# Optimization experiments

Hardware: AMD Instinct MI355X
Metric: run time of the kernel (lower is better)

Reference implementation:

```python
import jax, jax.numpy as jnp
import numpy as np

N_NODES = 100000
N_EDGES = 1250000
D_IN = 64
D_OUT = 64


def setup_inputs() -> dict:
    key = jax.random.key(0)
    k1, k2, k3, k4, k5, k6 = jax.random.split(key, 6)
    x = jax.random.normal(k1, (N_NODES, D_IN), dtype=jnp.float32)
    W_self = jax.random.normal(k2, (D_IN, D_OUT), dtype=jnp.float32) / np.sqrt(D_IN)
    W_neigh = jax.random.normal(k3, (D_IN, D_OUT), dtype=jnp.float32) / np.sqrt(D_IN)
    b = jax.random.normal(k4, (D_OUT,), dtype=jnp.float32) * 0.01
    src = jax.random.randint(k5, (N_EDGES,), 0, N_NODES, dtype=jnp.int32)
    dst = jnp.sort(jax.random.randint(k6, (N_EDGES,), 0, N_NODES, dtype=jnp.int32))
    return {"x": x, "W_self": W_self, "W_neigh": W_neigh, "b": b, "src": src, "dst": dst}


def reference(x, W_self, W_neigh, b, src, dst):
    # DGL SAGEConv (aggregator_type='mean'):
    #   h_neigh[v] = mean_{u in N(v)} x[u]   (0 if in-degree 0)
    #   out = x @ W_self + h_neigh @ W_neigh + b
    n_nodes = x.shape[0]
    msgs = x[src]  # [E, D_IN] gather of source features
    agg = jax.ops.segment_sum(msgs, dst, num_segments=n_nodes)  # [N, D_IN]
    deg = jax.ops.segment_sum(jnp.ones_like(dst, dtype=x.dtype), dst, num_segments=n_nodes)
    h_neigh = agg / jnp.maximum(deg, 1.0)[:, None]
    return x @ W_self + h_neigh @ W_neigh + b
```

## Files before the change

### kernel.cpp

```cpp
#include <hip/hip_runtime.h>
#include <hip/hip_fp16.h>

#define NN 100000
#define NE 1250000
#define D 64
#define NTILE 1563
#define NWID (NTILE * 4)

__device__ inline float2 cvt2(unsigned u) {
    __half2 h = __builtin_bit_cast(__half2, u);
    return __half22float2(h);
}
__device__ inline unsigned pack2(float a, float b) {
    __half2 h = __floats2half2_rn(a, b);
    return __builtin_bit_cast(unsigned, h);
}

__global__ __launch_bounds__(256) void k_rowptr(const int* __restrict__ dst,
                                                int* __restrict__ row_ptr) {
    const int i = blockIdx.x * 256 + threadIdx.x;
    if (i >= NE) return;
    const int d = dst[i];
    const int prev = (i == 0) ? -1 : dst[i - 1];
    for (int v = prev + 1; v <= d; ++v) row_ptr[v] = i;
    if (i == NE - 1) {
        for (int v = d + 1; v <= NN; ++v) row_ptr[v] = NE;
    }
}

__global__ __launch_bounds__(256) void k_gemm(const float* __restrict__ x,
                                              const float* __restrict__ Wself,
                                              const float* __restrict__ Wneigh,
                                              const float* __restrict__ b,
                                              float* __restrict__ z,
                                              __half* __restrict__ y) {
    const int lane = threadIdx.x & 63;
    const int wid = __builtin_amdgcn_readfirstlane(blockIdx.x * 4 + (threadIdx.x >> 6));
    if (wid >= NWID) return;
    const int tile = wid >> 2;
    const int sel = wid & 3;
    const int jh = (sel & 1) * 32;
    const float* __restrict__ W = (sel & 2) ? Wneigh : Wself;

    const int n = tile * 64 + lane;
    const int nc = (n < NN) ? n : (NN - 1);
    const float* __restrict__ xr = x + (size_t)nc * D;

    float acc[32];
    #pragma unroll
    for (int j = 0; j < 32; ++j) acc[j] = 0.0f;

    #pragma unroll 2
    for (int k4 = 0; k4 < D / 4; ++k4) {
        const float4 xv = *(const float4*)(xr + k4 * 4);
        const float xk[4] = {xv.x, xv.y, xv.z, xv.w};
        #pragma unroll
        for (int i = 0; i < 4; ++i) {
            const float* __restrict__ wr = W + (k4 * 4 + i) * D + jh;
            #pragma unroll
            for (int j = 0; j < 32; ++j) {
                acc[j] = fmaf(xk[i], wr[j], acc[j]);
            }
        }
    }

    if (n < NN) {
        if (sel & 2) {
            unsigned p[16];
            #pragma unroll
            for (int g = 0; g < 16; ++g) p[g] = pack2(acc[2 * g], acc[2 * g + 1]);
            uint4* __restrict__ yo = (uint4*)(y + (size_t)n * D + jh);
            #pragma unroll
            for (int g = 0; g < 4; ++g) {
                uint4 v;
                v.x = p[4 * g + 0]; v.y = p[4 * g + 1];
                v.z = p[4 * g + 2]; v.w = p[4 * g + 3];
                yo[g] = v;
            }
        } else {
            float* __restrict__ zo = z + (size_t)n * D + jh;
            const float* __restrict__ br = b + jh;
            #pragma unroll
            for (int g = 0; g < 8; ++g) {
                float4 v;
                v.x = acc[g * 4 + 0] + br[g * 4 + 0];
                v.y = acc[g * 4 + 1] + br[g * 4 + 1];
                v.z = acc[g * 4 + 2] + br[g * 4 + 2];
                v.w = acc[g * 4 + 3] + br[g * 4 + 3];
                *(float4*)(zo + g * 4) = v;
            }
        }
    }
}

__global__ __launch_bounds__(256) void k_aggr(const __half* __restrict__ y,
                                              const int* __restrict__ src,
                                              const int* __restrict__ row_ptr,
                                              float* __restrict__ out) {
    const int lane = threadIdx.x & 63;
    const int half = lane >> 5;
    const int w    = lane & 31;
    const int wid  = blockIdx.x * 4 + (threadIdx.x >> 6);
    const int v    = wid * 2 + half;
    if (v >= NN) return;

    const int lo = row_ptr[v];
    const int hi = row_ptr[v + 1];
    const int deg = hi - lo;

    float a0 = 0.0f, a1 = 0.0f;
    if (deg > 0) {
        const int last = hi - 1;
        int sv[4];
        #pragma unroll
        for (int u = 0; u < 4; ++u) sv[u] = src[min(lo + u, last)];
        for (int e = lo; e < hi; e += 4) {
            unsigned r[4];
            #pragma unroll
            for (int u = 0; u < 4; ++u)
                r[u] = *(const unsigned*)(y + (size_t)sv[u] * D + w * 2);
            const int en = e + 4;
            #pragma unroll
            for (int u = 0; u < 4; ++u) sv[u] = src[min(en + u, last)];
            #pragma unroll
            for (int u = 0; u < 4; ++u) {
                if (e + u < hi) {
                    const float2 f = cvt2(r[u]);
                    a0 += f.x; a1 += f.y;
                }
            }
        }
    }
    const float inv = (deg > 0) ? 1.0f / (float)deg : 0.0f;
    float2* op = (float2*)(out + (size_t)v * D + w * 2);
    float2 o = *op;
    o.x += a0 * inv;
    o.y += a1 * inv;
    *op = o;
}

extern "C" void kernel_launch(void* const* d_in, const int* in_sizes, int n_in,
                              void* d_out, int out_size, void* d_ws, size_t ws_size,
                              hipStream_t stream) {
    const float* x      = (const float*)d_in[0];
    const float* Wself  = (const float*)d_in[1];
    const float* Wneigh = (const float*)d_in[2];
    const float* b      = (const float*)d_in[3];
    const int*   src    = (const int*)d_in[4];
    const int*   dst    = (const int*)d_in[5];
    float* out = (float*)d_out;

    __half* y      = (__half*)d_ws;
    int*   row_ptr = (int*)((char*)d_ws + (size_t)NN * D * 2);

    k_rowptr<<<(NE + 255) / 256, 256, 0, stream>>>(dst, row_ptr);
    k_gemm<<<(NWID + 3) / 4, 256, 0, stream>>>(x, Wself, Wneigh, b, out, y);
    k_aggr<<<(NN + 7) / 8, 256, 0, stream>>>(y, src, row_ptr, out);
}
```

Measured before the change: 154.8 us.

## Use split-fp16 MFMA for dense projection with pre-packed weights

```diff
diff --git a/kernel.cpp b/kernel.cpp
--- a/kernel.cpp
+++ b/kernel.cpp
@@ -4,91 +4,104 @@
 #define NN 100000
 #define NE 1250000
 #define D 64
-#define NTILE 1563
-#define NWID (NTILE * 4)
+#define MT 6250
+#define RP_BLOCKS 4883
+
+typedef _Float16 h8 __attribute__((ext_vector_type(8)));
+typedef float f4 __attribute__((ext_vector_type(4)));
 
 __device__ inline float2 cvt2(unsigned u) {
     __half2 h = __builtin_bit_cast(__half2, u);
     return __half22float2(h);
 }
-__device__ inline unsigned pack2(float a, float b) {
-    __half2 h = __floats2half2_rn(a, b);
-    return __builtin_bit_cast(unsigned, h);
-}
 
-__global__ __launch_bounds__(256) void k_rowptr(const int* __restrict__ dst,
-                                                int* __restrict__ row_ptr) {
-    const int i = blockIdx.x * 256 + threadIdx.x;
-    if (i >= NE) return;
-    const int d = dst[i];
-    const int prev = (i == 0) ? -1 : dst[i - 1];
-    for (int v = prev + 1; v <= d; ++v) row_ptr[v] = i;
-    if (i == NE - 1) {
-        for (int v = d + 1; v <= NN; ++v) row_ptr[v] = NE;
+__global__ __launch_bounds__(256) void k_prep(const int* __restrict__ dst,
+                                              int* __restrict__ row_ptr,
+                                              const float* __restrict__ Ws,
+                                              const float* __restrict__ Wn,
+                                              __half* __restrict__ Wp) {
+    if (blockIdx.x < RP_BLOCKS) {
+        const int i = blockIdx.x * 256 + threadIdx.x;
+        if (i >= NE) return;
+        const int d = dst[i];
+        const int prev = (i == 0) ? -1 : dst[i - 1];
+        for (int v = prev + 1; v <= d; ++v) row_ptr[v] = i;
+        if (i == NE - 1) {
+            for (int v = d + 1; v <= NN; ++v) row_ptr[v] = NE;
+        }
+    } else {
+        const int id = (blockIdx.x - RP_BLOCKS) * 256 + threadIdx.x;
+        const int p = id >> 13;
+        const int r = id & 8191;
+        const int i = r & 7;
+        const int l = (r >> 3) & 63;
+        const int f = (r >> 9) & 1;
+        const int t = r >> 10;
+        const int k = f * 32 + ((l >> 4) * 8) + i;
+        const int c = (t & 3) * 16 + (l & 15);
+        const float v = ((t < 4) ? Ws : Wn)[k * D + c];
+        const _Float16 hi = (_Float16)v;
+        const _Float16 out = p ? (_Float16)(v - (float)hi) : hi;
+        Wp[p * 8192 + r] = __builtin_bit_cast(__half, out);
     }
 }
 
-__global__ __launch_bounds__(256) void k_gemm(const float* __restrict__ x,
-                                              const float* __restrict__ Wself,
-                                              const float* __restrict__ Wneigh,
-                                              const float* __restrict__ b,
-                                              float* __restrict__ z,
-                                              __half* __restrict__ y) {
+__global__ __launch_bounds__(256) void k_mm(const float* __restrict__ x,
+                                            const __half* __restrict__ Wp,
+                                            const float* __restrict__ b,
+                                            float* __restrict__ z,
+                                            __half* __restrict__ y) {
     const int lane = threadIdx.x & 63;
-    const int wid = __builtin_amdgcn_readfirstlane(blockIdx.x * 4 + (threadIdx.x >> 6));
-    if (wid >= NWID) return;
-    const int tile = wid >> 2;
-    const int sel = wid & 3;
-    const int jh = (sel & 1) * 32;
-    const float* __restrict__ W = (sel & 2) ? Wneigh : Wself;
+    const int mt = blockIdx.x * 4 + (threadIdx.x >> 6);
+    if (mt >= MT) return;
+    const int row = lane & 15;
+    const int kg = lane >> 4;
+    const float* __restrict__ xr = x + (size_t)(mt * 16 + row) * D + kg * 8;
 
-    const int n = tile * 64 + lane;
-    const int nc = (n < NN) ? n : (NN - 1);
-    const float* __restrict__ xr = x + (size_t)nc * D;
+    const float4 v0 = *(const float4*)(xr);
+    const float4 v1 = *(const float4*)(xr + 4);
+    const float4 v2 = *(const float4*)(xr + 32);
+    const float4 v3 = *(const float4*)(xr + 36);
 
-    float acc[32];
+    const float xf0[8] = {v0.x, v0.y, v0.z, v0.w, v1.x, v1.y, v1.z, v1.w};
+    const float xf1[8] = {v2.x, v2.y, v2.z, v2.w, v3.x, v3.y, v3.z, v3.w};
+    h8 ah0, al0, ah1, al1;
     #pragma unroll
-    for (int j = 0; j < 32; ++j) acc[j] = 0.0f;
-
-    #pragma unroll 2
-    for (int k4 = 0; k4 < D / 4; ++k4) {
-        const float4 xv = *(const float4*)(xr + k4 * 4);
-        const float xk[4] = {xv.x, xv.y, xv.z, xv.w};
-        #pragma unroll
-        for (int i = 0; i < 4; ++i) {
-            const float* __restrict__ wr = W + (k4 * 4 + i) * D + jh;
-            #pragma unroll
-            for (int j = 0; j < 32; ++j) {
-                acc[j] = fmaf(xk[i], wr[j], acc[j]);
-            }
-        }
+    for (int i = 0; i < 8; ++i) {
+        const _Float16 h0 = (_Float16)xf0[i];
+        ah0[i] = h0;
+        al0[i] = (_Float16)(xf0[i] - (float)h0);
+        const _Float16 h1 = (_Float16)xf1[i];
+        ah1[i] = h1;
+        al1[i] = (_Float16)(xf1[i] - (float)h1);
     }
 
-    if (n < NN) {
-        if (sel & 2) {
-            unsigned p[16];
+    const _Float16* __restrict__ wp = (const _Float16*)Wp;
+    #pragma unroll
+    for (int t = 0; t < 8; ++t) {
+        const h8 bh0 = *(const h8*)(wp + ((t * 2 + 0) * 64 + lane) * 8);
+        const h8 bh1 = *(const h8*)(wp + ((t * 2 + 1) * 64 + lane) * 8);
+        const h8 bl0 = *(const h8*)(wp + 8192 + ((t * 2 + 0) * 64 + lane) * 8);
+        const h8 bl1 = *(const h8*)(wp + 8192 + ((t * 2 + 1) * 64 + lane) * 8);
+        f4 acc = {0.f, 0.f, 0.f, 0.f};
+        acc = __builtin_amdgcn_mfma_f32_16x16x32_f16(al0, bh0, acc, 0, 0, 0);
+        acc = __builtin_amdgcn_mfma_f32_16x16x32_f16(al1, bh1, acc, 0, 0, 0);
+        acc = __builtin_amdgcn_mfma_f32_16x16x32_f16(ah0, bl0, acc, 0, 0, 0);
+        acc = __builtin_amdgcn_mfma_f32_16x16x32_f16(ah1, bl1, acc, 0, 0, 0);
+        acc = __builtin_amdgcn_mfma_f32_16x16x32_f16(ah0, bh0, acc, 0, 0, 0);
+        acc = __builtin_amdgcn_mfma_f32_16x16x32_f16(ah1, bh1, acc, 0, 0, 0);
+
+        const int col = (t & 3) * 16 + (lane & 15);
+        const int r0 = mt * 16 + kg * 4;
+        if (t < 4) {
+            const float bb = b[col];
             #pragma unroll
-            for (int g = 0; g < 16; ++g) p[g] = pack2(acc[2 * g], acc[2 * g + 1]);
-            uint4* __restrict__ yo = (uint4*)(y + (size_t)n * D + jh);
+            for (int reg = 0; reg < 4; ++reg)
+                z[(size_t)(r0 + reg) * D + col] = acc[reg] + bb;
+        } else {
             #pragma unroll
-            for (int g = 0; g < 4; ++g) {
-                uint4 v;
-                v.x = p[4 * g + 0]; v.y = p[4 * g + 1];
-                v.z = p[4 * g + 2]; v.w = p[4 * g + 3];
-                yo[g] = v;
-            }
-        } else {
-            float* __restrict__ zo = z + (size_t)n * D + jh;
-            const float* __restrict__ br = b + jh;
-            #pragma unroll
-            for (int g = 0; g < 8; ++g) {
-                float4 v;
-                v.x = acc[g * 4 + 0] + br[g * 4 + 0];
-                v.y = acc[g * 4 + 1] + br[g * 4 + 1];
-                v.z = acc[g * 4 + 2] + br[g * 4 + 2];
-                v.w = acc[g * 4 + 3] + br[g * 4 + 3];
-                *(float4*)(zo + g * 4) = v;
-            }
+            for (int reg = 0; reg < 4; ++reg)
+                y[(size_t)(r0 + reg) * D + col] = __float2half(acc[reg]);
         }
     }
 }
@@ -150,10 +163,13 @@
     const int*   dst    = (const int*)d_in[5];
     float* out = (float*)d_out;
 
-    __half* y      = (__half*)d_ws;
-    int*   row_ptr = (int*)((char*)d_ws + (size_t)NN * D * 2);
+    __half* y = (__half*)d_ws;
+    const size_t yb = (size_t)NN * D * 2;
+    int* row_ptr = (int*)((char*)d_ws + yb);
+    const size_t rpb = (((size_t)(NN + 1) * 4) + 15) & ~(size_t)15;
+    __half* Wp = (__half*)((char*)d_ws + yb + rpb);
 
-    k_rowptr<<<(NE + 255) / 256, 256, 0, stream>>>(dst, row_ptr);
-    k_gemm<<<(NWID + 3) / 4, 256, 0, stream>>>(x, Wself, Wneigh, b, out, y);
+    k_prep<<<RP_BLOCKS + 64, 256, 0, stream>>>(dst, row_ptr, Wself, Wneigh, Wp);
+    k_mm<<<(MT + 3) / 4, 256, 0, stream>>>(x, Wp, b, out, y);
     k_aggr<<<(NN + 7) / 8, 256, 0, stream>>>(y, src, row_ptr, out);
 }
```

Measured after the change: 139.0 us. -10.2%, faster.
